# Optimization experiments

Measured on AMD Instinct MI355X. Metric: run time of the kernel, lower is better.

## Reference

```python
import jax, jax.numpy as jnp
import numpy as np

B, N, C = 2, 2048, 768
H = 16
D = C // H  # head_dim = 48
SCALE = 1.0 / float(np.sqrt(D))


def setup_inputs() -> dict:
    key = jax.random.key(0)
    ks = jax.random.split(key, 5)
    x = jax.random.normal(ks[0], (B, N, C), dtype=jnp.float32)
    # torch nn.Linear weights are [out, in]; apply as x @ W.T
    qkv_w = jax.random.normal(ks[1], (3 * C, C), dtype=jnp.float32) * 0.02
    qkv_b = jax.random.normal(ks[2], (3 * C,), dtype=jnp.float32) * 0.02
    proj_w = jax.random.normal(ks[3], (C, C), dtype=jnp.float32) * 0.02
    proj_b = jax.random.normal(ks[4], (C,), dtype=jnp.float32) * 0.02
    return {"x": x, "qkv_w": qkv_w, "qkv_b": qkv_b, "proj_w": proj_w, "proj_b": proj_b}


def reference(x, qkv_w, qkv_b, proj_w, proj_b):
    # qkv: (B, N, 3C) -> (3, B, H, N, D)
    qkv = x @ qkv_w.T + qkv_b
    qkv = qkv.reshape(B, N, 3, H, D).transpose(2, 0, 3, 1, 4)
    q, k, v = qkv[0], qkv[1], qkv[2]
    # manual attention: full (B, H, N, N) score matrix, as in the original
    attn = jnp.einsum('bhqd,bhkd->bhqk', q, k) * SCALE
    attn = jax.nn.softmax(attn, axis=-1)
    # attn_drop with p=0.0 (eval / deterministic) is identity
    y = jnp.einsum('bhqk,bhkd->bhqd', attn, v)
    y = y.transpose(0, 2, 1, 3).reshape(B, N, C)
    return y @ proj_w.T + proj_b
```

## Files before the change

kernel.cpp:

```cpp
#include <hip/hip_runtime.h>

typedef short v8s __attribute__((ext_vector_type(8)));
typedef float v4f __attribute__((ext_vector_type(4)));
typedef unsigned short u16;

#define NSEQ 2048
#define CDIM 768
#define NH   16
#define DH   48
#define DP   64
#define MROWS 4096
#define N3C  2304
#define BH   32

#if __has_builtin(__builtin_amdgcn_exp2f)
#define EXP2(x) __builtin_amdgcn_exp2f(x)
#else
#define EXP2(x) exp2f(x)
#endif
#if __has_builtin(__builtin_amdgcn_rcpf)
#define RCP(x) __builtin_amdgcn_rcpf(x)
#else
#define RCP(x) (1.0f/(x))
#endif

__device__ __forceinline__ u16 f2bf(float f){
  unsigned u = __float_as_uint(f);
  u += 0x7FFFu + ((u>>16)&1u);
  return (u16)(u>>16);
}

__device__ __forceinline__ void load_lds16(const u16* g, u16* l){
  __builtin_amdgcn_global_load_lds((const __attribute__((address_space(1))) void*)g,
                                   (__attribute__((address_space(3))) void*)l, 16, 0, 0);
}

__global__ __launch_bounds__(256) void convert_bf16(const float* __restrict__ src, u16* __restrict__ dst, int n8){
  int i = blockIdx.x*256 + threadIdx.x;
  if (i >= n8) return;
  v4f f0 = ((const v4f*)src)[i*2];
  v4f f1 = ((const v4f*)src)[i*2+1];
  v8s o;
#pragma unroll
  for (int j = 0; j < 4; j++) ((u16*)&o)[j]   = f2bf(f0[j]);
#pragma unroll
  for (int j = 0; j < 4; j++) ((u16*)&o)[4+j] = f2bf(f1[j]);
  ((v8s*)dst)[i] = o;
}

__global__ __launch_bounds__(256) void zero_pads(u16* __restrict__ q, u16* __restrict__ k,
                                                 u16* __restrict__ v){
  int idx = blockIdx.x*256 + threadIdx.x;
  v8s z = (v8s){0,0,0,0,0,0,0,0};
  int r = idx >> 1, half = idx & 1;
  *(v8s*)(q + (size_t)r*DP + DH + half*8) = z;
  *(v8s*)(k + (size_t)r*DP + DH + half*8) = z;
  int bh = idx >> 12, i = idx & 4095;
  int row = i >> 8, off = i & 255;
  const short one = (short)0x3F80;
  v8s val = (row == 0) ? (v8s){one,one,one,one,one,one,one,one} : z;
  *(v8s*)(v + ((size_t)(bh*DP + DH + row))*NSEQ + off*8) = val;
}

__global__ __launch_bounds__(256) void qkv_gemm(const u16* __restrict__ x, const u16* __restrict__ w,
                                                const float* __restrict__ bias,
                                                u16* __restrict__ q, u16* __restrict__ k, u16* __restrict__ v){
  __shared__ __align__(16) u16 As[128*32];
  __shared__ __align__(16) u16 Bs[128*32];
  const int wave = threadIdx.x >> 6;
  const int lane = threadIdx.x & 63;
  const int l15  = lane & 15;
  const int quad = lane >> 4;
  const int wm = wave & 1, wn = wave >> 1;
  const int m0 = blockIdx.x*128, n0 = blockIdx.y*128;

  const int srow = lane >> 2;
  const int sg   = (lane & 3) ^ ((lane >> 3) & 3);
  const int sgoff = sg*8;

  v4f acc[4][4];
#pragma unroll
  for (int i = 0; i < 4; i++)
#pragma unroll
    for (int j = 0; j < 4; j++) acc[i][j] = (v4f){0.f,0.f,0.f,0.f};

  const int sig = (l15 >> 1) & 3;

  for (int kt = 0; kt < CDIM/32; kt++){
    const int k0 = kt*32;
    __syncthreads();
#pragma unroll
    for (int j = 0; j < 2; j++){
      int c = wave*2 + j;
      int r = c*16 + srow;
      load_lds16(x + (size_t)(m0 + r)*CDIM + k0 + sgoff, &As[c*512]);
      load_lds16(w + (size_t)(n0 + r)*CDIM + k0 + sgoff, &Bs[c*512]);
    }
    __syncthreads();

    v8s af[4], bf[4];
#pragma unroll
    for (int t = 0; t < 4; t++){
      int ra = wm*64 + t*16 + l15;
      af[t] = *(const v8s*)(&As[ra*32 + ((quad ^ sig)<<3)]);
      int rb = wn*64 + t*16 + l15;
      bf[t] = *(const v8s*)(&Bs[rb*32 + ((quad ^ sig)<<3)]);
    }
#pragma unroll
    for (int ti = 0; ti < 4; ti++)
#pragma unroll
      for (int tj = 0; tj < 4; tj++)
        acc[ti][tj] = __builtin_amdgcn_mfma_f32_16x16x32_bf16(af[ti], bf[tj], acc[ti][tj], 0, 0, 0);
  }

  const float QS = 0.2082540589f;
#pragma unroll
  for (int tj = 0; tj < 4; tj++){
    const int c = n0 + wn*64 + tj*16 + l15;
    const float bv = bias[c];
    const int t = c / CDIM;
    const int rem = c - t*CDIM;
    const int h = rem / DH;
    const int d = rem - h*DH;
#pragma unroll
    for (int ti = 0; ti < 4; ti++){
#pragma unroll
      for (int r = 0; r < 4; r++){
        int m = m0 + wm*64 + ti*16 + quad*4 + r;
        int b_ = m >> 11;
        int n  = m & (NSEQ-1);
        float val = acc[ti][tj][r] + bv;
        if (t == 0) val *= QS;
        u16 o  = f2bf(val);
        int bhn = b_*NH + h;
        if (t == 0)      q[((size_t)bhn*NSEQ + n)*DP + d] = o;
        else if (t == 1) k[((size_t)bhn*NSEQ + n)*DP + d] = o;
        else             v[((size_t)bhn*DP + d)*NSEQ + n] = o;
      }
    }
  }
}

__global__ __launch_bounds__(256) void attn(const u16* __restrict__ q, const u16* __restrict__ k,
                                            const u16* __restrict__ v, u16* __restrict__ y){
  __shared__ __align__(16) u16 Kl[64*64];
  __shared__ __align__(16) u16 Vl[64*64];
  __shared__ __align__(16) u16 Pl[4][16*64];
  const int bh = blockIdx.x;
  const int qt = blockIdx.y;
  const int wave = threadIdx.x >> 6;
  const int lane = threadIdx.x & 63;
  const int l15  = lane & 15;
  const int quad = lane >> 4;
  const u16* qb = q + (size_t)bh*NSEQ*DP;
  const u16* kb = k + (size_t)bh*NSEQ*DP;
  const u16* vb = v + (size_t)bh*DP*NSEQ;
  const int qm = qt*64 + wave*16;

  v8s qf[2];
#pragma unroll
  for (int ks = 0; ks < 2; ks++)
    qf[ks] = *(const v8s*)(qb + (size_t)(qm + l15)*DP + ks*32 + quad*8);

  v4f o[4];
#pragma unroll
  for (int i = 0; i < 4; i++) o[i] = (v4f){0.f,0.f,0.f,0.f};

  int pwoff[4][4];
#pragma unroll
  for (int nt = 0; nt < 4; nt++)
#pragma unroll
    for (int r = 0; r < 4; r++){
      int row = quad*4 + r;
      int col = nt*16 + l15;
      pwoff[nt][r] = row*64 + ((((col>>3) ^ (row&7))<<3) | (col&7));
    }

  for (int kt = 0; kt < NSEQ/64; kt++){
    __syncthreads();
    {
      const int t = threadIdx.x;
#pragma unroll
      for (int p = 0; p < 2; p++){
        int ci  = t + p*256;
        int row = ci >> 3;
        int off = ci & 7;
        v8s kd = *(const v8s*)(kb + (size_t)(kt*64 + row)*DP + off*8);
        *(v8s*)(&Kl[row*64 + ((off ^ (row&7))<<3)]) = kd;
        v8s vd = *(const v8s*)(vb + (size_t)row*NSEQ + kt*64 + off*8);
        *(v8s*)(&Vl[row*64 + ((off ^ (row&7))<<3)]) = vd;
      }
    }
    __syncthreads();

    v4f s[4];
#pragma unroll
    for (int nt = 0; nt < 4; nt++){
      s[nt] = (v4f){0.f,0.f,0.f,0.f};
#pragma unroll
      for (int ks = 0; ks < 2; ks++){
        int rrow = nt*16 + l15;
        v8s bf = *(const v8s*)(&Kl[rrow*64 + (((ks*4+quad) ^ (rrow&7))<<3)]);
        s[nt] = __builtin_amdgcn_mfma_f32_16x16x32_bf16(qf[ks], bf, s[nt], 0, 0, 0);
      }
    }

#pragma unroll
    for (int nt = 0; nt < 4; nt++)
#pragma unroll
      for (int r = 0; r < 4; r++)
        Pl[wave][pwoff[nt][r]] = f2bf(EXP2(s[nt][r]));

    v8s pa[2];
#pragma unroll
    for (int ks = 0; ks < 2; ks++){
      int ga = ks*4 + quad;
      pa[ks] = *(const v8s*)(&Pl[wave][l15*64 + ((ga ^ (l15&7))<<3)]);
    }
#pragma unroll
    for (int dt = 0; dt < 4; dt++){
#pragma unroll
      for (int ks = 0; ks < 2; ks++){
        int row = dt*16 + l15;
        v8s vf = *(const v8s*)(&Vl[row*64 + (((ks*4+quad) ^ (row&7))<<3)]);
        o[dt] = __builtin_amdgcn_mfma_f32_16x16x32_bf16(pa[ks], vf, o[dt], 0, 0, 0);
      }
    }
  }

  const int b_ = bh / NH, h = bh % NH;
#pragma unroll
  for (int r = 0; r < 4; r++){
    float lsum = __shfl(o[3][r], quad << 4);
    float inv  = RCP(lsum);
    int rowg = b_*NSEQ + qm + quad*4 + r;
#pragma unroll
    for (int dt = 0; dt < 3; dt++)
      y[(size_t)rowg*CDIM + h*DH + dt*16 + l15] = f2bf(o[dt][r]*inv);
  }
}

__global__ __launch_bounds__(256) void proj_gemm(const u16* __restrict__ y, const u16* __restrict__ w,
                                                 const float* __restrict__ bias, float* __restrict__ out){
  __shared__ __align__(16) u16 As[64*32];
  __shared__ __align__(16) u16 Bs[128*32];
  const int wave = threadIdx.x >> 6;
  const int lane = threadIdx.x & 63;
  const int l15  = lane & 15;
  const int quad = lane >> 4;
  const int wm = wave & 1, wn = wave >> 1;
  const int m0 = blockIdx.x*64, n0 = blockIdx.y*128;

  const int srow = lane >> 2;
  const int sg   = (lane & 3) ^ ((lane >> 3) & 3);
  const int sgoff = sg*8;

  v4f acc[2][4];
#pragma unroll
  for (int i = 0; i < 2; i++)
#pragma unroll
    for (int j = 0; j < 4; j++) acc[i][j] = (v4f){0.f,0.f,0.f,0.f};

  const int sig = (l15 >> 1) & 3;

  for (int kt = 0; kt < CDIM/32; kt++){
    const int k0 = kt*32;
    __syncthreads();
    {
      int rA = wave*16 + srow;
      load_lds16(y + (size_t)(m0 + rA)*CDIM + k0 + sgoff, &As[wave*512]);
#pragma unroll
      for (int j = 0; j < 2; j++){
        int c = wave*2 + j;
        int rB = c*16 + srow;
        load_lds16(w + (size_t)(n0 + rB)*CDIM + k0 + sgoff, &Bs[c*512]);
      }
    }
    __syncthreads();

    v8s af[2], bf[4];
#pragma unroll
    for (int t = 0; t < 2; t++){
      int ra = wm*32 + t*16 + l15;
      af[t] = *(const v8s*)(&As[ra*32 + ((quad ^ sig)<<3)]);
    }
#pragma unroll
    for (int t = 0; t < 4; t++){
      int rb = wn*64 + t*16 + l15;
      bf[t] = *(const v8s*)(&Bs[rb*32 + ((quad ^ sig)<<3)]);
    }
#pragma unroll
    for (int ti = 0; ti < 2; ti++)
#pragma unroll
      for (int tj = 0; tj < 4; tj++)
        acc[ti][tj] = __builtin_amdgcn_mfma_f32_16x16x32_bf16(af[ti], bf[tj], acc[ti][tj], 0, 0, 0);
  }

#pragma unroll
  for (int tj = 0; tj < 4; tj++){
    const int c = n0 + wn*64 + tj*16 + l15;
    const float bv = bias[c];
#pragma unroll
    for (int ti = 0; ti < 2; ti++){
#pragma unroll
      for (int r = 0; r < 4; r++){
        int m = m0 + wm*32 + ti*16 + quad*4 + r;
        out[(size_t)m*CDIM + c] = acc[ti][tj][r] + bv;
      }
    }
  }
}

extern "C" void kernel_launch(void* const* d_in, const int* in_sizes, int n_in,
                              void* d_out, int out_size, void* d_ws, size_t ws_size,
                              hipStream_t stream){
  const float* x      = (const float*)d_in[0];
  const float* qkv_w  = (const float*)d_in[1];
  const float* qkv_b  = (const float*)d_in[2];
  const float* proj_w = (const float*)d_in[3];
  const float* proj_b = (const float*)d_in[4];
  float* out = (float*)d_out;

  u16* xb  = (u16*)d_ws;
  u16* wb  = xb  + (size_t)MROWS*CDIM;
  u16* pwb = wb  + (size_t)N3C*CDIM;
  u16* q   = pwb + (size_t)CDIM*CDIM;
  u16* k   = q + (size_t)BH*NSEQ*DP;
  u16* v   = k + (size_t)BH*NSEQ*DP;
  u16* y   = v + (size_t)BH*NSEQ*DP;

  convert_bf16<<<dim3(MROWS*CDIM/8/256), dim3(256), 0, stream>>>(x,      xb,  MROWS*CDIM/8);
  convert_bf16<<<dim3(N3C*CDIM/8/256),  dim3(256), 0, stream>>>(qkv_w,  wb,  N3C*CDIM/8);
  convert_bf16<<<dim3(CDIM*CDIM/8/256), dim3(256), 0, stream>>>(proj_w, pwb, CDIM*CDIM/8);

  zero_pads<<<dim3(512), dim3(256), 0, stream>>>(q, k, v);
  qkv_gemm<<<dim3(MROWS/128, N3C/128), dim3(256), 0, stream>>>(xb, wb, qkv_b, q, k, v);
  attn<<<dim3(BH, NSEQ/64), dim3(256), 0, stream>>>(q, k, v, y);
  proj_gemm<<<dim3(MROWS/64, CDIM/128), dim3(256), 0, stream>>>(y, pwb, proj_b, out);
}
```

Baseline: 187.8 us.

## Double query rows per attention wave and merge bf16 conversion launches

The attention kernel now has each wave handle two 16-row query sub-tiles (128 query rows per block), so every K/V tile staged in LDS feeds twice as many MFMAs and global K/V traffic per query is halved. The grid along the sequence is halved to match, which leaves 512 blocks, and per-wave register and LDS use for P roughly doubles, which may lower occupancy. The three fp32-to-bf16 conversion kernels are also merged into one launch that relies on the output buffers being contiguous in the workspace.

```diff
diff --git a/kernel.cpp b/kernel.cpp
--- a/kernel.cpp
+++ b/kernel.cpp
@@ -35,11 +35,19 @@
                                    (__attribute__((address_space(3))) void*)l, 16, 0, 0);
 }
 
-__global__ __launch_bounds__(256) void convert_bf16(const float* __restrict__ src, u16* __restrict__ dst, int n8){
+#define XN8  (MROWS*CDIM/8)
+#define WN8  (N3C*CDIM/8)
+#define PN8  (CDIM*CDIM/8)
+__global__ __launch_bounds__(256) void convert_all(const float* __restrict__ x, const float* __restrict__ w,
+                                                   const float* __restrict__ pw, u16* __restrict__ dst){
   int i = blockIdx.x*256 + threadIdx.x;
-  if (i >= n8) return;
-  v4f f0 = ((const v4f*)src)[i*2];
-  v4f f1 = ((const v4f*)src)[i*2+1];
+  if (i >= XN8 + WN8 + PN8) return;
+  const float* src;
+  if (i < XN8)            src = x  + (size_t)i*8;
+  else if (i < XN8+WN8)   src = w  + (size_t)(i - XN8)*8;
+  else                    src = pw + (size_t)(i - XN8 - WN8)*8;
+  v4f f0 = ((const v4f*)src)[0];
+  v4f f1 = ((const v4f*)src)[1];
   v8s o;
 #pragma unroll
   for (int j = 0; j < 4; j++) ((u16*)&o)[j]   = f2bf(f0[j]);
@@ -145,7 +153,7 @@
                                             const u16* __restrict__ v, u16* __restrict__ y){
   __shared__ __align__(16) u16 Kl[64*64];
   __shared__ __align__(16) u16 Vl[64*64];
-  __shared__ __align__(16) u16 Pl[4][16*64];
+  __shared__ __align__(16) u16 Pl[4][32*64];
   const int bh = blockIdx.x;
   const int qt = blockIdx.y;
   const int wave = threadIdx.x >> 6;
@@ -155,16 +163,20 @@
   const u16* qb = q + (size_t)bh*NSEQ*DP;
   const u16* kb = k + (size_t)bh*NSEQ*DP;
   const u16* vb = v + (size_t)bh*DP*NSEQ;
-  const int qm = qt*64 + wave*16;
-
-  v8s qf[2];
-#pragma unroll
-  for (int ks = 0; ks < 2; ks++)
-    qf[ks] = *(const v8s*)(qb + (size_t)(qm + l15)*DP + ks*32 + quad*8);
-
-  v4f o[4];
-#pragma unroll
-  for (int i = 0; i < 4; i++) o[i] = (v4f){0.f,0.f,0.f,0.f};
+  const int qm = qt*128 + wave*32;
+
+  v8s qf[2][2];
+#pragma unroll
+  for (int si = 0; si < 2; si++)
+#pragma unroll
+    for (int ks = 0; ks < 2; ks++)
+      qf[si][ks] = *(const v8s*)(qb + (size_t)(qm + si*16 + l15)*DP + ks*32 + quad*8);
+
+  v4f o[2][4];
+#pragma unroll
+  for (int si = 0; si < 2; si++)
+#pragma unroll
+    for (int i = 0; i < 4; i++) o[si][i] = (v4f){0.f,0.f,0.f,0.f};
 
   int pwoff[4][4];
 #pragma unroll
@@ -193,50 +205,60 @@
     }
     __syncthreads();
 
-    v4f s[4];
+    v4f s[2][4];
 #pragma unroll
     for (int nt = 0; nt < 4; nt++){
-      s[nt] = (v4f){0.f,0.f,0.f,0.f};
+      s[0][nt] = (v4f){0.f,0.f,0.f,0.f};
+      s[1][nt] = (v4f){0.f,0.f,0.f,0.f};
 #pragma unroll
       for (int ks = 0; ks < 2; ks++){
         int rrow = nt*16 + l15;
         v8s bf = *(const v8s*)(&Kl[rrow*64 + (((ks*4+quad) ^ (rrow&7))<<3)]);
-        s[nt] = __builtin_amdgcn_mfma_f32_16x16x32_bf16(qf[ks], bf, s[nt], 0, 0, 0);
-      }
-    }
-
-#pragma unroll
-    for (int nt = 0; nt < 4; nt++)
-#pragma unroll
-      for (int r = 0; r < 4; r++)
-        Pl[wave][pwoff[nt][r]] = f2bf(EXP2(s[nt][r]));
-
-    v8s pa[2];
-#pragma unroll
-    for (int ks = 0; ks < 2; ks++){
-      int ga = ks*4 + quad;
-      pa[ks] = *(const v8s*)(&Pl[wave][l15*64 + ((ga ^ (l15&7))<<3)]);
-    }
+        s[0][nt] = __builtin_amdgcn_mfma_f32_16x16x32_bf16(qf[0][ks], bf, s[0][nt], 0, 0, 0);
+        s[1][nt] = __builtin_amdgcn_mfma_f32_16x16x32_bf16(qf[1][ks], bf, s[1][nt], 0, 0, 0);
+      }
+    }
+
+#pragma unroll
+    for (int si = 0; si < 2; si++)
+#pragma unroll
+      for (int nt = 0; nt < 4; nt++)
+#pragma unroll
+        for (int r = 0; r < 4; r++)
+          Pl[wave][si*1024 + pwoff[nt][r]] = f2bf(EXP2(s[si][nt][r]));
+
+    v8s pa[2][2];
+#pragma unroll
+    for (int si = 0; si < 2; si++)
+#pragma unroll
+      for (int ks = 0; ks < 2; ks++){
+        int ga = ks*4 + quad;
+        pa[si][ks] = *(const v8s*)(&Pl[wave][si*1024 + l15*64 + ((ga ^ (l15&7))<<3)]);
+      }
 #pragma unroll
     for (int dt = 0; dt < 4; dt++){
 #pragma unroll
       for (int ks = 0; ks < 2; ks++){
         int row = dt*16 + l15;
         v8s vf = *(const v8s*)(&Vl[row*64 + (((ks*4+quad) ^ (row&7))<<3)]);
-        o[dt] = __builtin_amdgcn_mfma_f32_16x16x32_bf16(pa[ks], vf, o[dt], 0, 0, 0);
+        o[0][dt] = __builtin_amdgcn_mfma_f32_16x16x32_bf16(pa[0][ks], vf, o[0][dt], 0, 0, 0);
+        o[1][dt] = __builtin_amdgcn_mfma_f32_16x16x32_bf16(pa[1][ks], vf, o[1][dt], 0, 0, 0);
       }
     }
   }
 
   const int b_ = bh / NH, h = bh % NH;
 #pragma unroll
-  for (int r = 0; r < 4; r++){
-    float lsum = __shfl(o[3][r], quad << 4);
-    float inv  = RCP(lsum);
-    int rowg = b_*NSEQ + qm + quad*4 + r;
-#pragma unroll
-    for (int dt = 0; dt < 3; dt++)
-      y[(size_t)rowg*CDIM + h*DH + dt*16 + l15] = f2bf(o[dt][r]*inv);
+  for (int si = 0; si < 2; si++){
+#pragma unroll
+    for (int r = 0; r < 4; r++){
+      float lsum = __shfl(o[si][3][r], quad << 4);
+      float inv  = RCP(lsum);
+      int rowg = b_*NSEQ + qm + si*16 + quad*4 + r;
+#pragma unroll
+      for (int dt = 0; dt < 3; dt++)
+        y[(size_t)rowg*CDIM + h*DH + dt*16 + l15] = f2bf(o[si][dt][r]*inv);
+    }
   }
 }
 
@@ -329,12 +351,9 @@
   u16* v   = k + (size_t)BH*NSEQ*DP;
   u16* y   = v + (size_t)BH*NSEQ*DP;
 
-  convert_bf16<<<dim3(MROWS*CDIM/8/256), dim3(256), 0, stream>>>(x,      xb,  MROWS*CDIM/8);
-  convert_bf16<<<dim3(N3C*CDIM/8/256),  dim3(256), 0, stream>>>(qkv_w,  wb,  N3C*CDIM/8);
-  convert_bf16<<<dim3(CDIM*CDIM/8/256), dim3(256), 0, stream>>>(proj_w, pwb, CDIM*CDIM/8);
-
+  convert_all<<<dim3((XN8+WN8+PN8+255)/256), dim3(256), 0, stream>>>(x, qkv_w, proj_w, xb);
   zero_pads<<<dim3(512), dim3(256), 0, stream>>>(q, k, v);
   qkv_gemm<<<dim3(MROWS/128, N3C/128), dim3(256), 0, stream>>>(xb, wb, qkv_b, q, k, v);
-  attn<<<dim3(BH, NSEQ/64), dim3(256), 0, stream>>>(q, k, v, y);
+  attn<<<dim3(BH, NSEQ/128), dim3(256), 0, stream>>>(q, k, v, y);
   proj_gemm<<<dim3(MROWS/64, CDIM/128), dim3(256), 0, stream>>>(y, pwb, proj_b, out);
 }
```

Result: slower. 200.3 us (+6.6%).

## Split attention over two key halves and fuse conversion/pad-zeroing kernels

Applied to the files above, without the earlier changes.

The attention kernel now gets a third grid dimension that splits the key sequence into two halves. Each block writes unnormalized fp32 partial outputs and row sums to a workspace, and a new finalize kernel adds the halves, normalizes and writes the bf16 result. The aim is to double the number of attention blocks for better GPU fill. In exchange it adds fp32 partial traffic and one more launch. Separately, the three bf16 conversion launches and the pad-zeroing launch are merged into one prep kernel to cut launch overhead.

```diff
diff --git a/kernel.cpp b/kernel.cpp
--- a/kernel.cpp
+++ b/kernel.cpp
@@ -1,6 +1,7 @@
 #include <hip/hip_runtime.h>
 
 typedef short v8s __attribute__((ext_vector_type(8)));
+typedef short v4s __attribute__((ext_vector_type(4)));
 typedef float v4f __attribute__((ext_vector_type(4)));
 typedef unsigned short u16;
 
@@ -35,31 +36,40 @@
                                    (__attribute__((address_space(3))) void*)l, 16, 0, 0);
 }
 
-__global__ __launch_bounds__(256) void convert_bf16(const float* __restrict__ src, u16* __restrict__ dst, int n8){
-  int i = blockIdx.x*256 + threadIdx.x;
-  if (i >= n8) return;
-  v4f f0 = ((const v4f*)src)[i*2];
-  v4f f1 = ((const v4f*)src)[i*2+1];
-  v8s o;
-#pragma unroll
-  for (int j = 0; j < 4; j++) ((u16*)&o)[j]   = f2bf(f0[j]);
-#pragma unroll
-  for (int j = 0; j < 4; j++) ((u16*)&o)[4+j] = f2bf(f1[j]);
-  ((v8s*)dst)[i] = o;
-}
-
-__global__ __launch_bounds__(256) void zero_pads(u16* __restrict__ q, u16* __restrict__ k,
-                                                 u16* __restrict__ v){
-  int idx = blockIdx.x*256 + threadIdx.x;
-  v8s z = (v8s){0,0,0,0,0,0,0,0};
-  int r = idx >> 1, half = idx & 1;
-  *(v8s*)(q + (size_t)r*DP + DH + half*8) = z;
-  *(v8s*)(k + (size_t)r*DP + DH + half*8) = z;
-  int bh = idx >> 12, i = idx & 4095;
-  int row = i >> 8, off = i & 255;
-  const short one = (short)0x3F80;
-  v8s val = (row == 0) ? (v8s){one,one,one,one,one,one,one,one} : z;
-  *(v8s*)(v + ((size_t)(bh*DP + DH + row))*NSEQ + off*8) = val;
+#define XN8  (MROWS*CDIM/8)
+#define WN8  (N3C*CDIM/8)
+#define PN8  (CDIM*CDIM/8)
+#define CONVB ((XN8+WN8+PN8)/256)
+__global__ __launch_bounds__(256) void prep(const float* __restrict__ x, const float* __restrict__ w,
+                                            const float* __restrict__ pw, u16* __restrict__ dst,
+                                            u16* __restrict__ q, u16* __restrict__ k, u16* __restrict__ v){
+  int bid = blockIdx.x;
+  if (bid < CONVB){
+    int i = bid*256 + threadIdx.x;
+    const float* src;
+    if (i < XN8)            src = x  + (size_t)i*8;
+    else if (i < XN8+WN8)   src = w  + (size_t)(i - XN8)*8;
+    else                    src = pw + (size_t)(i - XN8 - WN8)*8;
+    v4f f0 = ((const v4f*)src)[0];
+    v4f f1 = ((const v4f*)src)[1];
+    v8s o;
+#pragma unroll
+    for (int j = 0; j < 4; j++) ((u16*)&o)[j]   = f2bf(f0[j]);
+#pragma unroll
+    for (int j = 0; j < 4; j++) ((u16*)&o)[4+j] = f2bf(f1[j]);
+    ((v8s*)dst)[i] = o;
+  } else {
+    int idx = (bid - CONVB)*256 + threadIdx.x;
+    v8s z = (v8s){0,0,0,0,0,0,0,0};
+    int r = idx >> 1, half = idx & 1;
+    *(v8s*)(q + (size_t)r*DP + DH + half*8) = z;
+    *(v8s*)(k + (size_t)r*DP + DH + half*8) = z;
+    int bh = idx >> 12, i = idx & 4095;
+    int row = i >> 8, off = i & 255;
+    const short one = (short)0x3F80;
+    v8s val = (row == 0) ? (v8s){one,one,one,one,one,one,one,one} : z;
+    *(v8s*)(v + ((size_t)(bh*DP + DH + row))*NSEQ + off*8) = val;
+  }
 }
 
 __global__ __launch_bounds__(256) void qkv_gemm(const u16* __restrict__ x, const u16* __restrict__ w,
@@ -142,12 +152,14 @@
 }
 
 __global__ __launch_bounds__(256) void attn(const u16* __restrict__ q, const u16* __restrict__ k,
-                                            const u16* __restrict__ v, u16* __restrict__ y){
+                                            const u16* __restrict__ v,
+                                            float* __restrict__ oacc, float* __restrict__ lacc){
   __shared__ __align__(16) u16 Kl[64*64];
   __shared__ __align__(16) u16 Vl[64*64];
   __shared__ __align__(16) u16 Pl[4][16*64];
   const int bh = blockIdx.x;
   const int qt = blockIdx.y;
+  const int sp = blockIdx.z;
   const int wave = threadIdx.x >> 6;
   const int lane = threadIdx.x & 63;
   const int l15  = lane & 15;
@@ -176,7 +188,7 @@
       pwoff[nt][r] = row*64 + ((((col>>3) ^ (row&7))<<3) | (col&7));
     }
 
-  for (int kt = 0; kt < NSEQ/64; kt++){
+  for (int kt = sp*16; kt < sp*16 + 16; kt++){
     __syncthreads();
     {
       const int t = threadIdx.x;
@@ -229,15 +241,32 @@
   }
 
   const int b_ = bh / NH, h = bh % NH;
+  float* oa = oacc + (size_t)sp*MROWS*CDIM;
+  float* la = lacc + (size_t)sp*MROWS*NH;
 #pragma unroll
   for (int r = 0; r < 4; r++){
-    float lsum = __shfl(o[3][r], quad << 4);
-    float inv  = RCP(lsum);
     int rowg = b_*NSEQ + qm + quad*4 + r;
 #pragma unroll
     for (int dt = 0; dt < 3; dt++)
-      y[(size_t)rowg*CDIM + h*DH + dt*16 + l15] = f2bf(o[dt][r]*inv);
-  }
+      oa[(size_t)rowg*CDIM + h*DH + dt*16 + l15] = o[dt][r];
+    if (l15 == 0) la[rowg*NH + h] = o[3][r];
+  }
+}
+
+__global__ __launch_bounds__(256) void finalize(const float* __restrict__ oacc,
+                                                const float* __restrict__ lacc,
+                                                u16* __restrict__ y){
+  int i = blockIdx.x*256 + threadIdx.x;
+  int rowg = i / 192, c4 = i - rowg*192;
+  int c = c4*4, h = c / DH;
+  float l = lacc[rowg*NH + h] + lacc[MROWS*NH + rowg*NH + h];
+  float inv = RCP(l);
+  v4f a = *(const v4f*)(oacc + (size_t)rowg*CDIM + c);
+  v4f b = *(const v4f*)(oacc + (size_t)MROWS*CDIM + (size_t)rowg*CDIM + c);
+  v4s o4;
+#pragma unroll
+  for (int j = 0; j < 4; j++) o4[j] = (short)f2bf((a[j] + b[j])*inv);
+  *(v4s*)(y + (size_t)rowg*CDIM + c) = o4;
 }
 
 __global__ __launch_bounds__(256) void proj_gemm(const u16* __restrict__ y, const u16* __restrict__ w,
@@ -327,14 +356,13 @@
   u16* q   = pwb + (size_t)CDIM*CDIM;
   u16* k   = q + (size_t)BH*NSEQ*DP;
   u16* v   = k + (size_t)BH*NSEQ*DP;
-  u16* y   = v + (size_t)BH*NSEQ*DP;
-
-  convert_bf16<<<dim3(MROWS*CDIM/8/256), dim3(256), 0, stream>>>(x,      xb,  MROWS*CDIM/8);
-  convert_bf16<<<dim3(N3C*CDIM/8/256),  dim3(256), 0, stream>>>(qkv_w,  wb,  N3C*CDIM/8);
-  convert_bf16<<<dim3(CDIM*CDIM/8/256), dim3(256), 0, stream>>>(proj_w, pwb, CDIM*CDIM/8);
-
-  zero_pads<<<dim3(512), dim3(256), 0, stream>>>(q, k, v);
+  float* oacc = (float*)(v + (size_t)BH*NSEQ*DP);
+  float* lacc = oacc + (size_t)2*MROWS*CDIM;
+  u16* y = xb;
+
+  prep<<<dim3(CONVB + 512), dim3(256), 0, stream>>>(x, qkv_w, proj_w, xb, q, k, v);
   qkv_gemm<<<dim3(MROWS/128, N3C/128), dim3(256), 0, stream>>>(xb, wb, qkv_b, q, k, v);
-  attn<<<dim3(BH, NSEQ/64), dim3(256), 0, stream>>>(q, k, v, y);
+  attn<<<dim3(BH, NSEQ/64, 2), dim3(256), 0, stream>>>(q, k, v, oacc, lacc);
+  finalize<<<dim3(MROWS*192/256), dim3(256), 0, stream>>>(oacc, lacc, y);
   proj_gemm<<<dim3(MROWS/64, CDIM/128), dim3(256), 0, stream>>>(y, pwb, proj_b, out);
 }
```

After: 185.0 us. About the same (-1.5%).
